# Optimization experiments

Hardware: AMD Instinct MI355X
Metric: run time of the kernel (lower is better)

Reference implementation:

```python
import jax, jax.numpy as jnp
import numpy as np

D_MODEL = 1024
N_HEADS = 16
HEAD_DIM = D_MODEL // N_HEADS


def setup_inputs() -> dict:
    key = jax.random.key(0)
    k0, k1, k2, k3, k4, k5 = jax.random.split(key, 6)
    s = 1.0 / np.sqrt(D_MODEL)
    return {
        "q": jax.random.normal(k0, (2, 2048, D_MODEL), dtype=jnp.float32),
        "Wq": jax.random.normal(k1, (D_MODEL, D_MODEL), dtype=jnp.float32) * s,
        "Wk": jax.random.normal(k2, (D_MODEL, D_MODEL), dtype=jnp.float32) * s,
        "Wv": jax.random.normal(k3, (D_MODEL, D_MODEL), dtype=jnp.float32) * s,
        "Wo": jax.random.normal(k4, (D_MODEL, D_MODEL), dtype=jnp.float32) * s,
        "bo": jax.random.normal(k5, (D_MODEL,), dtype=jnp.float32) * 0.01,
    }


def _split_heads(x):
    b, s, _ = x.shape
    return x.reshape(b, s, N_HEADS, HEAD_DIM).transpose(0, 2, 1, 3)  # [b,h,s,d]


def reference(q, Wq, Wk, Wv, Wo, bo):
    # self-attention: k = v = q
    qh = _split_heads(q @ Wq)  # [b,h,s,d]
    kh = _split_heads(q @ Wk)
    vh = _split_heads(q @ Wv)
    scale = 1.0 / np.sqrt(HEAD_DIM).astype(np.float32)
    scores = jnp.einsum("bhqd,bhkd->bhqk", qh, kh) * scale
    attn = jax.nn.softmax(scores, axis=-1)
    ctx = jnp.einsum("bhqk,bhkd->bhqd", attn, vh)
    b, h, s, d = ctx.shape
    ctx = ctx.transpose(0, 2, 1, 3).reshape(b, s, h * d)
    return ctx @ Wo + bo
```

## Files before the change

### kernel.cpp

```cpp
#include <hip/hip_runtime.h>
#include <cstdint>

typedef unsigned short u16;
typedef __bf16 bf16x8 __attribute__((ext_vector_type(8)));
typedef __bf16 bf16x2 __attribute__((ext_vector_type(2)));
typedef float floatx4 __attribute__((ext_vector_type(4)));
typedef unsigned short u16x4 __attribute__((ext_vector_type(4)));
typedef unsigned short u16x8 __attribute__((ext_vector_type(8)));

#define MFMA16(a, b, c) __builtin_amdgcn_mfma_f32_16x16x32_bf16((a), (b), (c), 0, 0, 0)
#define QSCALE_LOG2E 0.18033688011112042f


typedef __attribute__((address_space(3))) void as3_void;
typedef __attribute__((address_space(1))) void as1_void;

static __device__ __forceinline__ void async_load16(const void* g, void* l) {
  __builtin_amdgcn_global_load_lds((as1_void*)(uintptr_t)g, (as3_void*)(uintptr_t)l,
                                   16, 0, 0);
}

static __device__ __forceinline__ u16 f2bf(float f) {
  union { float f; unsigned int u; } v; v.f = f;
  unsigned int u = v.u;
  u += 0x7fffu + ((u >> 16) & 1u);
  return (u16)(u >> 16);
}

static __device__ __forceinline__ u16x4 pack_bf4(float a, float b, float c, float d) {
#if __has_builtin(__builtin_amdgcn_cvt_pk_bf16_f32)
  union { u16x4 v4; bf16x2 v2[2]; } u;
  u.v2[0] = __builtin_amdgcn_cvt_pk_bf16_f32(a, b);
  u.v2[1] = __builtin_amdgcn_cvt_pk_bf16_f32(c, d);
  return u.v4;
#else
  u16x4 r; r[0] = f2bf(a); r[1] = f2bf(b); r[2] = f2bf(c); r[3] = f2bf(d);
  return r;
#endif
}

static __device__ __forceinline__ unsigned pack_bf2(float a, float b) {
#if __has_builtin(__builtin_amdgcn_cvt_pk_bf16_f32)
  union { bf16x2 v; unsigned u; } x;
  x.v = __builtin_amdgcn_cvt_pk_bf16_f32(a, b);
  return x.u;
#else
  return (unsigned)f2bf(a) | ((unsigned)f2bf(b) << 16);
#endif
}

static __device__ __forceinline__ float fast_exp2(float x) {
#if __has_builtin(__builtin_amdgcn_exp2f)
  return __builtin_amdgcn_exp2f(x);
#else
  return exp2f(x);
#endif
}


__global__ __launch_bounds__(256) void prep_kernel(
    const float* __restrict__ w0, const float* __restrict__ w1,
    const float* __restrict__ w2, const float* __restrict__ w3,
    u16* __restrict__ wout,
    const float* __restrict__ xin, u16* __restrict__ xout) {
  if (blockIdx.z == 4) {
    int blk = blockIdx.y * 16 + blockIdx.x;
    size_t base = (size_t)blk * 16384 + (size_t)threadIdx.x * 8;
#pragma unroll
    for (int r = 0; r < 8; r++) {
      size_t i = base + (size_t)r * 2048;
      float4 a = *(const float4*)(xin + i);
      float4 b = *(const float4*)(xin + i + 4);
      u16x8 o;
      o[0] = f2bf(a.x); o[1] = f2bf(a.y); o[2] = f2bf(a.z); o[3] = f2bf(a.w);
      o[4] = f2bf(b.x); o[5] = f2bf(b.y); o[6] = f2bf(b.z); o[7] = f2bf(b.w);
      *(u16x8*)(xout + i) = o;
    }
    return;
  }
  __shared__ u16 t[64][65];
  const float* in = (blockIdx.z == 0) ? w0 : (blockIdx.z == 1) ? w1
                    : (blockIdx.z == 2) ? w2 : w3;
  u16* oz = wout + (size_t)blockIdx.z * (1024 * 1024);
  const int tid = threadIdx.x;
  const int x = tid & 63, y0 = tid >> 6;
  const int bx = blockIdx.x * 64, by = blockIdx.y * 64;
#pragma unroll
  for (int p = 0; p < 16; p++) {
    int y = y0 + p * 4;
    t[y][x] = f2bf(in[(size_t)(by + y) * 1024 + bx + x]);
  }
  __syncthreads();
#pragma unroll
  for (int p = 0; p < 16; p++) {
    int r = y0 + p * 4;
    oz[(size_t)(bx + r) * 1024 + by + x] = t[x][r];
  }
}


__global__ __launch_bounds__(256, 3) void gemm_qkv_kernel(
    const u16* __restrict__ A, const u16* __restrict__ BT,
    u16* __restrict__ out, u16* __restrict__ outVT) {
  __shared__ __align__(16) u16 sm[2 * 4096 + 2 * 4096];
  u16* As = sm;
  u16* Bs = sm + 2 * 4096;
  u16* tb = sm;
  const int tid = threadIdx.x;
  const int w = tid >> 6, lane = tid & 63;
  const int bm = blockIdx.y * 128, bn = blockIdx.x * 128;
  const int z = blockIdx.z;
  const int K = 1024, N = 1024;
  const u16* Bz = BT + (size_t)z * N * K;

  const int c0 = w * 2, c1 = c0 + 1;
  const int mA0 = c0 * 16 + (lane >> 2), mA1 = c1 * 16 + (lane >> 2);
  const int kg0 = (lane & 3) ^ ((mA0 >> 1) & 3);
  const int kg1 = (lane & 3) ^ ((mA1 >> 1) & 3);
  const u16* agp0 = A + (size_t)(bm + mA0) * K + kg0 * 8;
  const u16* agp1 = A + (size_t)(bm + mA1) * K + kg1 * 8;
  const u16* bgp0 = Bz + (size_t)(bn + mA0) * K + kg0 * 8;
  const u16* bgp1 = Bz + (size_t)(bn + mA1) * K + kg1 * 8;

  const int wm = (w >> 1) * 64, wn = (w & 1) * 64;
  floatx4 acc[4][4] = {};

  int a_off[4], b_off[4];
#pragma unroll
  for (int i = 0; i < 4; i++) {
    int m = wm + i * 16 + (lane & 15);
    a_off[i] = m * 32 + (((lane >> 4) ^ ((m >> 1) & 3)) * 8);
    int n = wn + i * 16 + (lane & 15);
    b_off[i] = n * 32 + (((lane >> 4) ^ ((n >> 1) & 3)) * 8);
  }

  auto issueQ = [&](int buf, int k0) {
    u16* ab = As + buf * 4096;
    u16* bb = Bs + buf * 4096;
    async_load16(agp0 + k0, ab + c0 * 512);
    async_load16(agp1 + k0, ab + c1 * 512);
    async_load16(bgp0 + k0, bb + c0 * 512);
    async_load16(bgp1 + k0, bb + c1 * 512);
  };

  issueQ(0, 0);
  asm volatile("s_waitcnt vmcnt(0)" ::: "memory");
  __builtin_amdgcn_s_barrier();

#pragma unroll 2
  for (int kk = 0; kk < 32; ++kk) {
    if (kk < 31) issueQ((kk + 1) & 1, (kk + 1) * 32);
    const u16* Ab = As + (kk & 1) * 4096;
    const u16* Bb = Bs + (kk & 1) * 4096;
    bf16x8 af[4], bf[4];
#pragma unroll
    for (int i = 0; i < 4; i++) af[i] = *(const bf16x8*)(Ab + a_off[i]);
#pragma unroll
    for (int j = 0; j < 4; j++) bf[j] = *(const bf16x8*)(Bb + b_off[j]);
    __builtin_amdgcn_s_setprio(1);
#pragma unroll
    for (int i = 0; i < 4; i++)
#pragma unroll
      for (int j = 0; j < 4; j++)
        acc[i][j] = MFMA16(af[i], bf[j], acc[i][j]);
    __builtin_amdgcn_s_setprio(0);
    asm volatile("s_waitcnt vmcnt(0) lgkmcnt(0)" ::: "memory");
    __builtin_amdgcn_s_barrier();
  }

  const int roff = (lane >> 4) * 4;
  const int coff = lane & 15;
  if (z == 2) {
    const int b = bm >> 11, s0 = bm & 2047;
#pragma unroll
    for (int half = 0; half < 2; half++) {
      __syncthreads();
      if ((w & 1) == half) {
#pragma unroll
        for (int i = 0; i < 4; i++) {
          int s_local = wm + i * 16 + roff;
#pragma unroll
          for (int j = 0; j < 4; j++) {
            int c_local = j * 16 + coff;
            u16x4 pk = pack_bf4(acc[i][j][0], acc[i][j][1],
                                acc[i][j][2], acc[i][j][3]);
            *(u16x4*)(tb + c_local * 136 + s_local) = pk;
          }
        }
      }
      __syncthreads();
#pragma unroll
      for (int p = 0; p < 4; p++) {
        int c_local = (tid >> 4) & 15;
        int row = p * 16 + c_local;
        int so = tid & 15;
        int cg = bn + half * 64 + row;
        int h = cg >> 6, d = cg & 63;
        u16x8 vv = *(const u16x8*)(tb + row * 136 + so * 8);
        *(u16x8*)(outVT + ((size_t)(b * 16 + h) * 64 + d) * 2048 + s0 + so * 8) = vv;
      }
    }
  } else {
    const float sc = (z == 0) ? QSCALE_LOG2E : 1.0f;
    u16* outz = out + (size_t)z * 4096 * 1024;
#pragma unroll
    for (int i = 0; i < 4; i++) {
      int r0 = bm + wm + i * 16 + roff;
#pragma unroll
      for (int j = 0; j < 4; j++) {
        int c = bn + wn + j * 16 + coff;
#pragma unroll
        for (int r = 0; r < 4; r++)
          outz[(size_t)(r0 + r) * N + c] = f2bf(acc[i][j][r] * sc);
      }
    }
  }
}


__global__ __launch_bounds__(256, 2) void gemm_o_kernel(
    const u16* __restrict__ A, const u16* __restrict__ BT,
    const float* __restrict__ bias, float* __restrict__ out) {
  __shared__ u16 As[2 * 4096];
  __shared__ u16 Bs[2 * 2048];
  const int tid = threadIdx.x;
  const int w = tid >> 6, lane = tid & 63;
  const int bm = blockIdx.y * 128, bn = blockIdx.x * 64;
  const int K = 1024, N = 1024;

  const u16* gp[3];
  u16* ldp[2][3];
#pragma unroll
  for (int i = 0; i < 3; i++) {
    int c = w * 3 + i;
    if (c < 8) {
      int m = c * 16 + (lane >> 2);
      int kg = (lane & 3) ^ ((m >> 1) & 3);
      gp[i] = A + (size_t)(bm + m) * K + kg * 8;
      ldp[0][i] = As + c * 512;
      ldp[1][i] = As + 4096 + c * 512;
    } else {
      int cb = c - 8;
      int n = cb * 16 + (lane >> 2);
      int kg = (lane & 3) ^ ((n >> 1) & 3);
      gp[i] = BT + (size_t)(bn + n) * K + kg * 8;
      ldp[0][i] = Bs + cb * 512;
      ldp[1][i] = Bs + 2048 + cb * 512;
    }
  }

  const int wm = (w >> 1) * 64, wn = (w & 1) * 32;
  floatx4 acc[4][2] = {};

  int a_off[4], b_off[2];
#pragma unroll
  for (int i = 0; i < 4; i++) {
    int m = wm + i * 16 + (lane & 15);
    a_off[i] = m * 32 + (((lane >> 4) ^ ((m >> 1) & 3)) * 8);
  }
#pragma unroll
  for (int j = 0; j < 2; j++) {
    int n = wn + j * 16 + (lane & 15);
    b_off[j] = n * 32 + (((lane >> 4) ^ ((n >> 1) & 3)) * 8);
  }

  auto issueO = [&](int buf, int k0) {
#pragma unroll
    for (int i = 0; i < 3; i++)
      async_load16(gp[i] + k0, buf ? ldp[1][i] : ldp[0][i]);
  };

  issueO(0, 0);
  asm volatile("s_waitcnt vmcnt(0)" ::: "memory");
  __builtin_amdgcn_s_barrier();

#pragma unroll 2
  for (int kk = 0; kk < 32; ++kk) {
    if (kk < 31) issueO((kk + 1) & 1, (kk + 1) * 32);
    const u16* Ab = As + (kk & 1) * 4096;
    const u16* Bb = Bs + (kk & 1) * 2048;
    bf16x8 af[4], bf[2];
#pragma unroll
    for (int i = 0; i < 4; i++) af[i] = *(const bf16x8*)(Ab + a_off[i]);
#pragma unroll
    for (int j = 0; j < 2; j++) bf[j] = *(const bf16x8*)(Bb + b_off[j]);
    __builtin_amdgcn_s_setprio(1);
#pragma unroll
    for (int i = 0; i < 4; i++)
#pragma unroll
      for (int j = 0; j < 2; j++)
        acc[i][j] = MFMA16(af[i], bf[j], acc[i][j]);
    __builtin_amdgcn_s_setprio(0);
    asm volatile("s_waitcnt vmcnt(0) lgkmcnt(0)" ::: "memory");
    __builtin_amdgcn_s_barrier();
  }

  const int roff = (lane >> 4) * 4;
  const int coff = lane & 15;
#pragma unroll
  for (int i = 0; i < 4; i++) {
    int r0 = bm + wm + i * 16 + roff;
#pragma unroll
    for (int j = 0; j < 2; j++) {
      int c = bn + wn + j * 16 + coff;
      float bv = bias[c];
#pragma unroll
      for (int r = 0; r < 4; r++)
        out[(size_t)(r0 + r) * N + c] = acc[i][j][r] + bv;
    }
  }
}


__global__ __launch_bounds__(512, 4) void attn_kernel(
    const u16* __restrict__ Q, const u16* __restrict__ Kx,
    const u16* __restrict__ VT, u16* __restrict__ ctx) {
  __shared__ __align__(16) u16 lds[32768];
  const int tid = threadIdx.x;
  const int w = tid >> 6, lane = tid & 63;
  const int qq = w >> 1, sh = w & 1;
  const int quad = lane >> 4;
  const int bid = blockIdx.x;
  const int bh = (bid >> 7) * 8 + (bid & 7);
  const int q0 = ((bid >> 3) & 15) * 128;
  const int b = bh >> 4, h = bh & 15;
  const u16* Qh = Q + (size_t)b * 2048 * 1024 + h * 64;
  const u16* Kh = Kx + (size_t)b * 2048 * 1024 + h * 64;
  const u16* Vh = VT + (size_t)bh * 64 * 2048;

  const u16* kgp[2]; const u16* vgp[2];
  int kc[2], vc[2];
#pragma unroll
  for (int i = 0; i < 2; i++) {
    int c = w * 2 + i;
    int sl = c * 8 + (lane >> 3);
    int dg = (lane & 7) ^ (lane >> 3);
    kgp[i] = Kh + (size_t)sl * 1024 + dg * 8;
    kc[i] = c * 512;
    int dl = c * 4 + quad;
    int sg = (lane & 15) ^ (dl & 15);
    vgp[i] = Vh + (size_t)dl * 2048 + sg * 8;
    vc[i] = 8192 + c * 512;
  }

  auto issue_tile = [&](int buf, int t) {
    u16* dst = lds + buf * 16384;
    const size_t k0 = (size_t)t * 128;
#pragma unroll
    for (int i = 0; i < 2; i++) {
      async_load16(kgp[i] + k0 * 1024, dst + kc[i]);
      async_load16(vgp[i] + k0, dst + vc[i]);
    }
  };

  issue_tile(0, 0);

  const int qbase = q0 + qq * 32;
  bf16x8 qf[2][2];
#pragma unroll
  for (int qt = 0; qt < 2; qt++)
#pragma unroll
    for (int ks = 0; ks < 2; ks++)
      qf[qt][ks] = *(const bf16x8*)(Qh + (size_t)(qbase + qt * 16 + (lane & 15)) * 1024 +
                                    ks * 32 + quad * 8);

  bf16x8 onesf;
#pragma unroll
  for (int i = 0; i < 8; i++) onesf[i] = (__bf16)1.0f;
  const floatx4 zero4 = {};

  const int slot_k0 = quad ^ (lane & 7);
  const int slot_k1 = (4 + quad) ^ (lane & 7);
  const int koff0 = sh * 4096 + (lane & 15) * 64 + slot_k0 * 8;
  const int koff1 = sh * 4096 + (lane & 15) * 64 + slot_k1 * 8;
  const int sq = ((quad & 1) << 1) | (quad >> 1);

  floatx4 o[2][4] = {};
  floatx4 lacc[2] = {};

  asm volatile("s_waitcnt vmcnt(0)" ::: "memory");

#pragma unroll 2
  for (int t = 0; t < 16; ++t) {
    __builtin_amdgcn_s_barrier();
    __builtin_amdgcn_sched_barrier(0);
    if (t < 15) issue_tile((t + 1) & 1, t + 1);
    const u16* Ksb = lds + (t & 1) * 16384;
    const u16* Vsb = Ksb + 8192;

    floatx4 st[4][2];
    __builtin_amdgcn_s_setprio(1);
#pragma unroll
    for (int si = 0; si < 4; si++) {
      bf16x8 kf0 = *(const bf16x8*)(Ksb + koff0 + si * 1024);
      bf16x8 kf1 = *(const bf16x8*)(Ksb + koff1 + si * 1024);
#pragma unroll
      for (int qt = 0; qt < 2; qt++)
        st[si][qt] = MFMA16(kf1, qf[qt][1], MFMA16(kf0, qf[qt][0], zero4));
    }
    __builtin_amdgcn_s_setprio(0);

    unsigned pa[2][4], pb[2][4];
#pragma unroll
    for (int si = 0; si < 4; si++)
#pragma unroll
      for (int qt = 0; qt < 2; qt++) {
        pa[qt][si] = pack_bf2(fast_exp2(st[si][qt][0]), fast_exp2(st[si][qt][1]));
        pb[qt][si] = pack_bf2(fast_exp2(st[si][qt][2]), fast_exp2(st[si][qt][3]));
      }

    bf16x8 pf[2][2];
#pragma unroll
    for (int qt = 0; qt < 2; qt++)
#pragma unroll
      for (int ksl = 0; ksl < 2; ksl++) {
        unsigned x0 = pa[qt][2 * ksl], x1 = pa[qt][2 * ksl + 1];
        unsigned y0 = pb[qt][2 * ksl], y1 = pb[qt][2 * ksl + 1];
        asm("v_permlane16_swap_b32 %0, %1" : "+v"(x0), "+v"(x1));
        asm("v_permlane16_swap_b32 %0, %1" : "+v"(y0), "+v"(y1));
        union { unsigned u[4]; bf16x8 v; } uu;
        uu.u[0] = x0; uu.u[1] = y0; uu.u[2] = x1; uu.u[3] = y1;
        pf[qt][ksl] = uu.v;
      }

    __builtin_amdgcn_s_setprio(1);
#pragma unroll
    for (int ksl = 0; ksl < 2; ksl++) {
      int kb = sh * 2 + ksl;
      bf16x8 vf[4];
#pragma unroll
      for (int jt = 0; jt < 4; jt++) {
        int d = jt * 16 + (lane & 15);
        int slot = (kb * 4 + sq) ^ (d & 15);
        vf[jt] = *(const bf16x8*)(Vsb + d * 128 + slot * 8);
      }
#pragma unroll
      for (int qt = 0; qt < 2; qt++) {
#pragma unroll
        for (int jt = 0; jt < 4; jt++)
          o[qt][jt] = MFMA16(pf[qt][ksl], vf[jt], o[qt][jt]);
        lacc[qt] = MFMA16(pf[qt][ksl], onesf, lacc[qt]);
      }
    }
    __builtin_amdgcn_s_setprio(0);
    asm volatile("s_waitcnt vmcnt(0)" ::: "memory");
  }

  __syncthreads();
  floatx4* dump  = (floatx4*)lds;
  floatx4* ldump = (floatx4*)(lds + 16384);
  if (sh == 1) {
    int base = qq * 512;
#pragma unroll
    for (int qt = 0; qt < 2; qt++)
#pragma unroll
      for (int jt = 0; jt < 4; jt++)
        dump[base + (qt * 4 + jt) * 64 + lane] = o[qt][jt];
#pragma unroll
    for (int qt = 0; qt < 2; qt++)
      ldump[qq * 128 + qt * 64 + lane] = lacc[qt];
  }
  __syncthreads();
  if (sh == 0) {
    int base = qq * 512;
#pragma unroll
    for (int qt = 0; qt < 2; qt++)
#pragma unroll
      for (int jt = 0; jt < 4; jt++)
        o[qt][jt] += dump[base + (qt * 4 + jt) * 64 + lane];
#pragma unroll
    for (int qt = 0; qt < 2; qt++)
      lacc[qt] += ldump[qq * 128 + qt * 64 + lane];
#pragma unroll
    for (int qt = 0; qt < 2; qt++)
#pragma unroll
      for (int r = 0; r < 4; r++) {
        float inv = 1.0f / lacc[qt][r];
        int s = qbase + qt * 16 + quad * 4 + r;
#pragma unroll
        for (int j = 0; j < 4; j++) {
          int c = h * 64 + j * 16 + (lane & 15);
          ctx[(size_t)(b * 2048 + s) * 1024 + c] = f2bf(o[qt][j][r] * inv);
        }
      }
  }
}


extern "C" void kernel_launch(void* const* d_in, const int* in_sizes, int n_in,
                              void* d_out, int out_size, void* d_ws, size_t ws_size,
                              hipStream_t stream) {
  (void)in_sizes; (void)n_in; (void)out_size; (void)ws_size;
  const float* x  = (const float*)d_in[0];
  const float* Wq = (const float*)d_in[1];
  const float* Wk = (const float*)d_in[2];
  const float* Wv = (const float*)d_in[3];
  const float* Wo = (const float*)d_in[4];
  const float* bo = (const float*)d_in[5];
  u16* ws = (u16*)d_ws;
  const size_t MM = 1024 * 1024;
  u16* WT  = ws;
  u16* WoT = ws + 3 * MM;
  u16* Xb  = ws + 4 * MM;
  u16* QKV = ws + 8 * MM;
  u16* VTp = ws + 20 * MM;
  u16* CTX = ws + 24 * MM;

  dim3 blk(256);
  prep_kernel<<<dim3(16, 16, 5), blk, 0, stream>>>(Wq, Wk, Wv, Wo, WT, x, Xb);
  gemm_qkv_kernel<<<dim3(8, 32, 3), blk, 0, stream>>>(Xb, WT, QKV, VTp);
  attn_kernel<<<dim3(512, 1, 1), dim3(512), 0, stream>>>(QKV, QKV + 4 * MM, VTp, CTX);
  gemm_o_kernel<<<dim3(16, 32, 1), blk, 0, stream>>>(CTX, WoT, bo, (float*)d_out);
}
```

Measured before the change: 178.3 us.

## Fuse Q/K/V projections into one GEMM sharing the A tile

The QKV GEMM now computes all three projections in one block: each block loads a 128-row A tile once and three 64-column B tiles (Wq, Wk, Wv), accumulating into three accumulator sets. This cuts the repeated A loads that the separate z-indexed launches made, and changes the grid from 8x32x3 with 128x128 tiles to 16x32 with 128x(3x64) tiles. In exchange it uses more registers and LDS (occupancy hint drops from 3 to 2), and every block now runs both the direct Q/K store and the transposed V epilogue.

```diff
diff --git a/kernel.cpp b/kernel.cpp
--- a/kernel.cpp
+++ b/kernel.cpp
@@ -99,48 +99,56 @@
 }
 
 
-__global__ __launch_bounds__(256, 3) void gemm_qkv_kernel(
+__global__ __launch_bounds__(256, 2) void gemm_qkv_kernel(
     const u16* __restrict__ A, const u16* __restrict__ BT,
     u16* __restrict__ out, u16* __restrict__ outVT) {
-  __shared__ __align__(16) u16 sm[2 * 4096 + 2 * 4096];
-  u16* As = sm;
-  u16* Bs = sm + 2 * 4096;
-  u16* tb = sm;
+  __shared__ __align__(16) u16 sm[2 * 10240];
+  __shared__ __align__(16) u16 tb2[64 * 72];
   const int tid = threadIdx.x;
   const int w = tid >> 6, lane = tid & 63;
-  const int bm = blockIdx.y * 128, bn = blockIdx.x * 128;
-  const int z = blockIdx.z;
+  const int bm = blockIdx.y * 128, bn = blockIdx.x * 64;
   const int K = 1024, N = 1024;
-  const u16* Bz = BT + (size_t)z * N * K;
-
-  const int c0 = w * 2, c1 = c0 + 1;
-  const int mA0 = c0 * 16 + (lane >> 2), mA1 = c1 * 16 + (lane >> 2);
-  const int kg0 = (lane & 3) ^ ((mA0 >> 1) & 3);
-  const int kg1 = (lane & 3) ^ ((mA1 >> 1) & 3);
-  const u16* agp0 = A + (size_t)(bm + mA0) * K + kg0 * 8;
-  const u16* agp1 = A + (size_t)(bm + mA1) * K + kg1 * 8;
-  const u16* bgp0 = Bz + (size_t)(bn + mA0) * K + kg0 * 8;
-  const u16* bgp1 = Bz + (size_t)(bn + mA1) * K + kg1 * 8;
-
-  const int wm = (w >> 1) * 64, wn = (w & 1) * 64;
-  floatx4 acc[4][4] = {};
-
-  int a_off[4], b_off[4];
+
+  const u16* gp[5];
+  int lo[5];
+#pragma unroll
+  for (int i = 0; i < 5; i++) {
+    int c = w * 5 + i;
+    if (c < 8) {
+      int m = c * 16 + (lane >> 2);
+      int kg = (lane & 3) ^ ((m >> 1) & 3);
+      gp[i] = A + (size_t)(bm + m) * K + kg * 8;
+      lo[i] = c * 512;
+    } else {
+      int cz = c - 8;
+      int z = cz >> 2;
+      int n = (cz & 3) * 16 + (lane >> 2);
+      int kg = (lane & 3) ^ ((n >> 1) & 3);
+      gp[i] = BT + (size_t)z * N * K + (size_t)(bn + n) * K + kg * 8;
+      lo[i] = 4096 + cz * 512;
+    }
+  }
+
+  const int wm = (w >> 1) * 64, wn = (w & 1) * 32;
+  floatx4 acc[3][4][2] = {};
+
+  int a_off[4], b_off[2];
 #pragma unroll
   for (int i = 0; i < 4; i++) {
     int m = wm + i * 16 + (lane & 15);
     a_off[i] = m * 32 + (((lane >> 4) ^ ((m >> 1) & 3)) * 8);
-    int n = wn + i * 16 + (lane & 15);
-    b_off[i] = n * 32 + (((lane >> 4) ^ ((n >> 1) & 3)) * 8);
+  }
+#pragma unroll
+  for (int j = 0; j < 2; j++) {
+    int n = wn + j * 16 + (lane & 15);
+    b_off[j] = n * 32 + (((lane >> 4) ^ ((n >> 1) & 3)) * 8);
   }
 
   auto issueQ = [&](int buf, int k0) {
-    u16* ab = As + buf * 4096;
-    u16* bb = Bs + buf * 4096;
-    async_load16(agp0 + k0, ab + c0 * 512);
-    async_load16(agp1 + k0, ab + c1 * 512);
-    async_load16(bgp0 + k0, bb + c0 * 512);
-    async_load16(bgp1 + k0, bb + c1 * 512);
+    u16* base = sm + buf * 10240;
+#pragma unroll
+    for (int i = 0; i < 5; i++)
+      async_load16(gp[i] + k0, base + lo[i]);
   };
 
   issueQ(0, 0);
@@ -150,19 +158,23 @@
 #pragma unroll 2
   for (int kk = 0; kk < 32; ++kk) {
     if (kk < 31) issueQ((kk + 1) & 1, (kk + 1) * 32);
-    const u16* Ab = As + (kk & 1) * 4096;
-    const u16* Bb = Bs + (kk & 1) * 4096;
-    bf16x8 af[4], bf[4];
+    const u16* Ab = sm + (kk & 1) * 10240;
+    bf16x8 af[4];
 #pragma unroll
     for (int i = 0; i < 4; i++) af[i] = *(const bf16x8*)(Ab + a_off[i]);
-#pragma unroll
-    for (int j = 0; j < 4; j++) bf[j] = *(const bf16x8*)(Bb + b_off[j]);
     __builtin_amdgcn_s_setprio(1);
 #pragma unroll
-    for (int i = 0; i < 4; i++)
-#pragma unroll
-      for (int j = 0; j < 4; j++)
-        acc[i][j] = MFMA16(af[i], bf[j], acc[i][j]);
+    for (int z = 0; z < 3; z++) {
+      const u16* Bb = Ab + 4096 + z * 2048;
+      bf16x8 bf[2];
+#pragma unroll
+      for (int j = 0; j < 2; j++) bf[j] = *(const bf16x8*)(Bb + b_off[j]);
+#pragma unroll
+      for (int i = 0; i < 4; i++)
+#pragma unroll
+        for (int j = 0; j < 2; j++)
+          acc[z][i][j] = MFMA16(af[i], bf[j], acc[z][i][j]);
+    }
     __builtin_amdgcn_s_setprio(0);
     asm volatile("s_waitcnt vmcnt(0) lgkmcnt(0)" ::: "memory");
     __builtin_amdgcn_s_barrier();
@@ -170,49 +182,51 @@
 
   const int roff = (lane >> 4) * 4;
   const int coff = lane & 15;
-  if (z == 2) {
-    const int b = bm >> 11, s0 = bm & 2047;
-#pragma unroll
-    for (int half = 0; half < 2; half++) {
-      __syncthreads();
-      if ((w & 1) == half) {
-#pragma unroll
-        for (int i = 0; i < 4; i++) {
-          int s_local = wm + i * 16 + roff;
-#pragma unroll
-          for (int j = 0; j < 4; j++) {
-            int c_local = j * 16 + coff;
-            u16x4 pk = pack_bf4(acc[i][j][0], acc[i][j][1],
-                                acc[i][j][2], acc[i][j][3]);
-            *(u16x4*)(tb + c_local * 136 + s_local) = pk;
-          }
-        }
-      }
-      __syncthreads();
-#pragma unroll
-      for (int p = 0; p < 4; p++) {
-        int c_local = (tid >> 4) & 15;
-        int row = p * 16 + c_local;
-        int so = tid & 15;
-        int cg = bn + half * 64 + row;
-        int h = cg >> 6, d = cg & 63;
-        u16x8 vv = *(const u16x8*)(tb + row * 136 + so * 8);
-        *(u16x8*)(outVT + ((size_t)(b * 16 + h) * 64 + d) * 2048 + s0 + so * 8) = vv;
-      }
-    }
-  } else {
+
+#pragma unroll
+  for (int z = 0; z < 2; z++) {
     const float sc = (z == 0) ? QSCALE_LOG2E : 1.0f;
     u16* outz = out + (size_t)z * 4096 * 1024;
 #pragma unroll
     for (int i = 0; i < 4; i++) {
       int r0 = bm + wm + i * 16 + roff;
 #pragma unroll
-      for (int j = 0; j < 4; j++) {
+      for (int j = 0; j < 2; j++) {
         int c = bn + wn + j * 16 + coff;
 #pragma unroll
         for (int r = 0; r < 4; r++)
-          outz[(size_t)(r0 + r) * N + c] = f2bf(acc[i][j][r] * sc);
-      }
+          outz[(size_t)(r0 + r) * N + c] = f2bf(acc[z][i][j][r] * sc);
+      }
+    }
+  }
+
+  const int b = bm >> 11, s0 = bm & 2047;
+#pragma unroll
+  for (int ha = 0; ha < 2; ha++) {
+    __syncthreads();
+    if ((w >> 1) == ha) {
+#pragma unroll
+      for (int i = 0; i < 4; i++) {
+        int s_l = i * 16 + roff;
+#pragma unroll
+        for (int j = 0; j < 2; j++) {
+          int c_local = wn + j * 16 + coff;
+          u16x4 pk = pack_bf4(acc[2][i][j][0], acc[2][i][j][1],
+                              acc[2][i][j][2], acc[2][i][j][3]);
+          *(u16x4*)(tb2 + c_local * 72 + s_l) = pk;
+        }
+      }
+    }
+    __syncthreads();
+#pragma unroll
+    for (int p = 0; p < 2; p++) {
+      int row = p * 32 + (tid >> 3);
+      int so = tid & 7;
+      int cg = bn + row;
+      int h = cg >> 6, d = cg & 63;
+      u16x8 vv = *(const u16x8*)(tb2 + row * 72 + so * 8);
+      *(u16x8*)(outVT + ((size_t)(b * 16 + h) * 64 + d) * 2048 +
+                s0 + ha * 64 + so * 8) = vv;
     }
   }
 }
@@ -508,7 +522,7 @@
 
   dim3 blk(256);
   prep_kernel<<<dim3(16, 16, 5), blk, 0, stream>>>(Wq, Wk, Wv, Wo, WT, x, Xb);
-  gemm_qkv_kernel<<<dim3(8, 32, 3), blk, 0, stream>>>(Xb, WT, QKV, VTp);
+  gemm_qkv_kernel<<<dim3(16, 32, 1), blk, 0, stream>>>(Xb, WT, QKV, VTp);
   attn_kernel<<<dim3(512, 1, 1), dim3(512), 0, stream>>>(QKV, QKV + 4 * MM, VTp, CTX);
   gemm_o_kernel<<<dim3(16, 32, 1), blk, 0, stream>>>(CTX, WoT, bo, (float*)d_out);
 }
```

New measurement: 176.1 us. About the same (-1.2%).
